# Kernel tuning notes

Measured on AMD Instinct MI355X. Metric: run time of the kernel, lower is better.

## Reference

```python
import jax, jax.numpy as jnp
import numpy as np

IN_DIM = 512
OUT_DIM = 512


def setup_inputs() -> dict:
    key = jax.random.key(0)
    ks = jax.random.split(key, 7)
    B, S = 4, 2048
    scale = 1.0 / np.sqrt(IN_DIM)
    X = jax.random.normal(ks[0], (B, S, IN_DIM), dtype=jnp.float32)
    Wq = jax.random.normal(ks[1], (IN_DIM, OUT_DIM), dtype=jnp.float32) * scale
    Wk = jax.random.normal(ks[2], (IN_DIM, OUT_DIM), dtype=jnp.float32) * scale
    Wv = jax.random.normal(ks[3], (IN_DIM, OUT_DIM), dtype=jnp.float32) * scale
    bq = jnp.zeros((OUT_DIM,), dtype=jnp.float32)
    bk = jnp.zeros((OUT_DIM,), dtype=jnp.float32)
    bv = jnp.zeros((OUT_DIM,), dtype=jnp.float32)
    return {"X": X, "Wq": Wq, "bq": bq, "Wk": Wk, "bk": bk, "Wv": Wv, "bv": bv}


def reference(X, Wq, bq, Wk, bk, Wv, bv):
    # Q/K/V projections: [B,S,in] @ [in,out] -> [B,S,out]
    Q = X @ Wq + bq
    K = X @ Wk + bk
    V = X @ Wv + bv
    d_k = jnp.asarray(Q.shape[-1], Q.dtype)
    # scores: [B,S,S] = QK^T / sqrt(d_k)
    scores = jnp.einsum('bsd,btd->bst', Q, K) / jnp.sqrt(d_k)
    attn = jax.nn.softmax(scores, axis=-1)
    # out: [B,S,out]
    return jnp.einsum('bst,btd->bsd', attn, V)
```

## Files before the change

kernel.cpp:

```cpp
#include <hip/hip_runtime.h>
#include <hip/hip_bf16.h>
#include <stdint.h>

#define SEQ   2048
#define DIM   512
#define BATCH 4

typedef __attribute__((ext_vector_type(8))) short  short8;
typedef __attribute__((ext_vector_type(4))) float  floatx4;

static __device__ __forceinline__ unsigned short f2b(float f) {
  return __builtin_bit_cast(unsigned short, __float2bfloat16(f));
}

static __device__ __forceinline__ void gll16(const void* g, void* l) {
  __builtin_amdgcn_global_load_lds(
      (__attribute__((address_space(1))) void*)(uintptr_t)g,
      (__attribute__((address_space(3))) void*)l, 16, 0, 0);
}


template <int AF, int BF, int WM, int WN, int KC, int PH, int KIT, int NW>
__device__ __forceinline__ void fgemm_p(
    const char* __restrict__ A, int rtA0, int TKA,
    const char* __restrict__ B, int rtB0, int TKB,
    char* lds, floatx4 (&acc)[AF / WM][BF / WN])
{
  constexpr int AWF  = AF / WM, BWF = BF / WN;
  constexpr int SLOT = (AF + BF) * KC * 1024;
  constexpr int L    = KC * (AF / NW + BF / NW);
  constexpr int AC   = AWF / PH;
  static_assert(KIT >= 3, "pipeline needs >=3 K-slots");
  static_assert(AF % NW == 0 && BF % NW == 0, "frag rows must divide waves");
  static_assert(AWF % PH == 0 && L % PH == 0, "phase split must divide");
  const int tid = threadIdx.x;
  const int w = tid >> 6, l = tid & 63;
  const int wm = w % WM, wn = w / WM;

  auto stage_part = [&](char* dst, int kt, int p) {
#pragma unroll
    for (int g = p * (L / PH); g < (p + 1) * (L / PH); ++g) {
      if (g < KC * (AF / NW)) {
        const int c = g / (AF / NW), q = g % (AF / NW);
        const int f = q * NW + w;
        gll16(A + (((size_t)(rtA0 + f) * TKA + kt * KC + c) << 10) + l * 16,
              dst + (c * AF + f) * 1024 + l * 16);
      } else {
        const int h = g - KC * (AF / NW);
        const int c = h / (BF / NW), q = h % (BF / NW);
        const int f = q * NW + w;
        gll16(B + (((size_t)(rtB0 + f) * TKB + kt * KC + c) << 10) + l * 16,
              dst + (KC * AF + c * BF + f) * 1024 + l * 16);
      }
    }
  };

#pragma unroll
  for (int p = 0; p < PH; ++p) stage_part(lds, 0, p);
#pragma unroll
  for (int p = 0; p < PH; ++p) stage_part(lds + SLOT, 1, p);
  asm volatile("s_waitcnt vmcnt(%0) lgkmcnt(0)\ns_barrier" :: "n"(L) : "memory");

  short8 bf[KC][BWF];
  int cs = 0;
#pragma unroll 2
  for (int kt = 0; kt < KIT; ++kt) {
    const char* bA = lds + cs * SLOT;
    const char* bB = bA + KC * AF * 1024;
    int ns = cs - 1; if (ns < 0) ns = 2;
    char* pdst = lds + ns * SLOT;
#pragma unroll
    for (int p = 0; p < PH; ++p) {
      short8 af[KC][AC];
#pragma unroll
      for (int c = 0; c < KC; ++c)
#pragma unroll
        for (int i = 0; i < AC; ++i)
          af[c][i] = *(const short8*)(bA + (c * AF + wm * AWF + p * AC + i) * 1024 + l * 16);
      if (p == 0) {
#pragma unroll
        for (int c = 0; c < KC; ++c)
#pragma unroll
          for (int j = 0; j < BWF; ++j)
            bf[c][j] = *(const short8*)(bB + (c * BF + wn * BWF + j) * 1024 + l * 16);
      }
      if (kt + 2 < KIT) stage_part(pdst, kt + 2, p);

      asm volatile("s_barrier" ::: "memory");
      asm volatile("s_waitcnt lgkmcnt(0)" ::: "memory");
      __builtin_amdgcn_s_setprio(1);
#pragma unroll
      for (int c = 0; c < KC; ++c)
#pragma unroll
        for (int i = 0; i < AC; ++i)
#pragma unroll
          for (int j = 0; j < BWF; ++j)
            acc[p * AC + i][j] = __builtin_amdgcn_mfma_f32_16x16x32_bf16(
                af[c][i], bf[c][j], acc[p * AC + i][j], 0, 0, 0);
      __builtin_amdgcn_s_setprio(0);

      if (p == PH - 1) {
        if (kt + 2 < KIT)
          asm volatile("s_waitcnt vmcnt(%0)\ns_barrier" :: "n"(L) : "memory");
        else if (kt + 1 < KIT)
          asm volatile("s_waitcnt vmcnt(0)\ns_barrier" ::: "memory");
      } else {
        asm volatile("s_barrier" ::: "memory");
      }
    }
    ++cs; if (cs == 3) cs = 0;
  }
}

__global__ __launch_bounds__(256) void setup_kernel(
    const float* __restrict__ X, const float* __restrict__ Wq,
    const float* __restrict__ Wk, const float* __restrict__ Wv,
    short8* __restrict__ XbF, short8* __restrict__ WF)
{
  const int flat = blockIdx.x * 256 + threadIdx.x;
  {
    const int tile = flat >> 6, l = flat & 63;
    const int row = (tile >> 4) * 16 + (l & 15);
    const int k0  = (tile & 15) * 32 + (l >> 4) * 8;
    const float4 v0 = *(const float4*)(X + (size_t)row * DIM + k0);
    const float4 v1 = *(const float4*)(X + (size_t)row * DIM + k0 + 4);
    short8 o;
    o[0] = (short)f2b(v0.x); o[1] = (short)f2b(v0.y);
    o[2] = (short)f2b(v0.z); o[3] = (short)f2b(v0.w);
    o[4] = (short)f2b(v1.x); o[5] = (short)f2b(v1.y);
    o[6] = (short)f2b(v1.z); o[7] = (short)f2b(v1.w);
    XbF[flat] = o;
  }
  if (flat < 3 * 32768) {
    const int z = flat >> 15, within = flat & 32767;
    const float* W = (z == 0) ? Wq : (z == 1) ? Wk : Wv;
    const int tile = within >> 6, l = within & 63;
    const int n  = (tile >> 4) * 16 + (l & 15);
    const int k0 = (tile & 15) * 32 + (l >> 4) * 8;
    short8 o;
#pragma unroll
    for (int e = 0; e < 8; ++e)
      o[e] = (short)f2b(W[(size_t)(k0 + e) * DIM + n]);
    WF[flat] = o;
  }
}

__global__ __launch_bounds__(256, 2) void qkv_kernel(
    const short8* __restrict__ XbF, const short8* __restrict__ WF,
    const float* __restrict__ bq, const float* __restrict__ bk,
    const float* __restrict__ bv,
    unsigned short* __restrict__ QF, unsigned short* __restrict__ KF,
    unsigned short* __restrict__ VF)
{
  __shared__ char lds[73728];
  const int blk = blockIdx.x;
  const int n = (blk & 7) * 48 + (blk >> 3);
  const int lane = threadIdx.x & 63, w = threadIdx.x >> 6;
  const int wm = w & 1, wn = w >> 1;
  const char* Xc = (const char*)XbF;
  const char* Wc = (const char*)WF;
  floatx4 acc[8][4] = {};

  if (n < 256) {
    const int z = n >> 7, y = (n >> 6) & 1, x = n & 63;
    fgemm_p<16, 8, 2, 2, 1, 2, 16, 4>(Wc + (size_t)z * 524288, y * 16, 16,
                                      Xc, x * 8, 16, lds, acc);
    const float* bias = z ? bk : bq;
    unsigned short* OF = z ? KF : QF;
    const int dbase = y * 256 + wm * 128;
    const int sbase = x * 128 + wn * 64;
#pragma unroll
    for (int i2 = 0; i2 < 8; ++i2) {
      const int d0 = dbase + i2 * 16 + (lane >> 4) * 4;
      const float4 b4 = *(const float4*)(bias + d0);
#pragma unroll
      for (int j = 0; j < 4; ++j) {
        const int s = sbase + j * 16 + (lane & 15);
        ushort4 pk;
        pk.x = f2b(acc[i2][j][0] + b4.x);
        pk.y = f2b(acc[i2][j][1] + b4.y);
        pk.z = f2b(acc[i2][j][2] + b4.z);
        pk.w = f2b(acc[i2][j][3] + b4.w);
        *(ushort4*)(OF + (size_t)((s >> 4) * 16 + (d0 >> 5)) * 512 +
                    ((((d0 & 31) >> 3) << 4) | (s & 15)) * 8 + (d0 & 7)) = pk;
      }
    }
  } else {
    const int m = n - 256;
    const int x = m >> 2, y = m & 3;
    fgemm_p<16, 8, 2, 2, 1, 2, 16, 4>(Xc, x * 16, 16,
                                      Wc + 2 * 524288, y * 8, 16, lds, acc);
    const int sbase = x * 256 + wm * 128;
    const int dbase = y * 128 + wn * 64;
#pragma unroll
    for (int i2 = 0; i2 < 8; ++i2) {
      const int s0 = sbase + i2 * 16 + (lane >> 4) * 4;
      const int bt = s0 >> 11, t0 = s0 & 2047;
#pragma unroll
      for (int j = 0; j < 4; ++j) {
        const int d = dbase + j * 16 + (lane & 15);
        const float bn = bv[d];
        ushort4 pk;
        pk.x = f2b(acc[i2][j][0] + bn);
        pk.y = f2b(acc[i2][j][1] + bn);
        pk.z = f2b(acc[i2][j][2] + bn);
        pk.w = f2b(acc[i2][j][3] + bn);
        *(ushort4*)(VF + (size_t)bt * DIM * SEQ +
                    (size_t)((d >> 4) * 64 + (t0 >> 5)) * 512 +
                    ((((t0 & 31) >> 3) << 4) | (d & 15)) * 8 + (t0 & 7)) = pk;
      }
    }
  }
}

__global__ __launch_bounds__(256, 2) void scores_kernel(
    const unsigned short* __restrict__ QF, const unsigned short* __restrict__ KF,
    unsigned short* __restrict__ ScF, float* __restrict__ prow)
{
  __shared__ char lds[73728];
  const int blk = blockIdx.x;
  const int n = (blk & 7) * 64 + (blk >> 3);
  const int b = n >> 7, t = n & 127;
  const int y = t >> 4, x = t & 15;
  const int lane = threadIdx.x & 63, w = threadIdx.x >> 6;
  const int wm = w & 1, wn = w >> 1;
  floatx4 acc[8][4] = {};
  fgemm_p<16, 8, 2, 2, 1, 2, 16, 4>((const char*)KF + (size_t)b * 2097152, y * 16, 16,
                                    (const char*)QF + (size_t)b * 2097152, x * 8, 16,
                                    lds, acc);

  unsigned short* S = ScF + (size_t)b * SEQ * SEQ;
  const float scale = 0.044194173824159216f;
  const int tbase = y * 256 + wm * 128;
  const int sbase = x * 128 + wn * 64;
  float colsum[4] = {0.f, 0.f, 0.f, 0.f};
#pragma unroll
  for (int i2 = 0; i2 < 8; ++i2) {
    const int t0 = tbase + i2 * 16 + (lane >> 4) * 4;
#pragma unroll
    for (int j = 0; j < 4; ++j) {
      const int s = sbase + j * 16 + (lane & 15);
      float e0 = __expf(acc[i2][j][0] * scale);
      float e1 = __expf(acc[i2][j][1] * scale);
      float e2 = __expf(acc[i2][j][2] * scale);
      float e3 = __expf(acc[i2][j][3] * scale);
      colsum[j] += (e0 + e1) + (e2 + e3);
      ushort4 pk;
      pk.x = f2b(e0); pk.y = f2b(e1); pk.z = f2b(e2); pk.w = f2b(e3);
      *(ushort4*)(S + (size_t)((s >> 4) * 64 + (t0 >> 5)) * 512 +
                  ((((t0 & 31) >> 3) << 4) | (s & 15)) * 8 + (t0 & 7)) = pk;
    }
  }
#pragma unroll
  for (int j = 0; j < 4; ++j) {
    colsum[j] += __shfl_xor(colsum[j], 16, 64);
    colsum[j] += __shfl_xor(colsum[j], 32, 64);
  }
  if (lane < 16) {
    float* dst = prow + ((size_t)(y * 2 + wm) * BATCH + b) * SEQ + sbase + lane;
#pragma unroll
    for (int j = 0; j < 4; ++j) dst[j * 16] = colsum[j];
  }
}

__global__ __launch_bounds__(256, 2) void pv_kernel(
    const unsigned short* __restrict__ ScF, const unsigned short* __restrict__ VF,
    const float* __restrict__ prow, float* __restrict__ out)
{
  __shared__ char lds[73728];
  __shared__ float rinv[128];
  const int blk = blockIdx.x;
  const int n = (blk & 7) * 64 + (blk >> 3);
  const int b = n >> 7, r = n & 127;
  const int x = r >> 3, y = r & 7;
  const int t = threadIdx.x;
  if (t < 128) {
    const int s = x * 128 + t;
    float rr = 0.f;
#pragma unroll
    for (int q = 0; q < 16; ++q) rr += prow[((size_t)q * BATCH + b) * SEQ + s];
    rinv[t] = 1.f / rr;
  }
  const int lane = threadIdx.x & 63, w = threadIdx.x >> 6;
  const int wm = w & 1, wn = w >> 1;
  floatx4 acc[4][2] = {};
  fgemm_p<8, 4, 2, 2, 2, 1, 32, 4>((const char*)ScF + (size_t)b * 8388608, x * 8, 64,
                                   (const char*)VF + (size_t)b * 2097152, y * 4, 64,
                                   lds, acc);

  const int mbase = x * 128 + wm * 64;
  const int dbase = y * 64 + wn * 32;
#pragma unroll
  for (int i2 = 0; i2 < 4; ++i2) {
    const int r0 = wm * 64 + i2 * 16 + (lane >> 4) * 4;
    const int m0 = mbase + i2 * 16 + (lane >> 4) * 4;
    const float inv0 = rinv[r0], inv1 = rinv[r0 + 1], inv2 = rinv[r0 + 2], inv3 = rinv[r0 + 3];
#pragma unroll
    for (int j = 0; j < 2; ++j) {
      const int d = dbase + j * 16 + (lane & 15);
      float* o = out + ((size_t)b * SEQ + m0) * DIM + d;
      o[0 * DIM] = acc[i2][j][0] * inv0;
      o[1 * DIM] = acc[i2][j][1] * inv1;
      o[2 * DIM] = acc[i2][j][2] * inv2;
      o[3 * DIM] = acc[i2][j][3] * inv3;
    }
  }
}

extern "C" void kernel_launch(void* const* d_in, const int* in_sizes, int n_in,
                              void* d_out, int out_size, void* d_ws, size_t ws_size,
                              hipStream_t stream) {
  const float* X  = (const float*)d_in[0];
  const float* Wq = (const float*)d_in[1];
  const float* bq = (const float*)d_in[2];
  const float* Wk = (const float*)d_in[3];
  const float* bk = (const float*)d_in[4];
  const float* Wv = (const float*)d_in[5];
  const float* bv = (const float*)d_in[6];
  float* out = (float*)d_out;
  char* ws = (char*)d_ws;

  short8* XbF = (short8*)(ws + 0);
  float*  prow = (float*)(ws + 0);
  short8* WF  = (short8*)(ws + 8388608);
  unsigned short* QF  = (unsigned short*)(ws + 9961472);
  unsigned short* KF  = (unsigned short*)(ws + 18350080);
  unsigned short* VF  = (unsigned short*)(ws + 26738688);
  unsigned short* ScF = (unsigned short*)(ws + 35127296);

  setup_kernel<<<dim3(2048), 256, 0, stream>>>(X, Wq, Wk, Wv, XbF, WF);
  qkv_kernel<<<dim3(384), 256, 0, stream>>>(XbF, WF, bq, bk, bv, QF, KF, VF);
  scores_kernel<<<dim3(512), 256, 0, stream>>>(QF, KF, ScF, prow);
  pv_kernel<<<dim3(512), 256, 0, stream>>>(ScF, VF, prow, out);
}
```

Before: 137.7 us.

## Use eight-wave blocks in all GEMM kernels with per-slot staging

Doubles the waves per block from 4 to 8 in the QKV, scores and PV kernels by splitting the N dimension of each block tile across four wave columns instead of two, which halves each wave's accumulator tile. Staging is restructured so that each wave issues one contiguous share of a whole K slot, all during the first phase, instead of splitting loads across phases. The aim is more waves to hide latency and lower register pressure per wave. The cost is more redundant LDS reads of the A fragments per block, a heavier burst of global loads in phase 0, and an occupancy gain that may be capped by the 72KB of LDS each block uses.

```diff
diff --git a/kernel.cpp b/kernel.cpp
--- a/kernel.cpp
+++ b/kernel.cpp
@@ -21,45 +21,43 @@
 
 
 template <int AF, int BF, int WM, int WN, int KC, int PH, int KIT, int NW>
-__device__ __forceinline__ void fgemm_p(
+__device__ __forceinline__ void fgemm_v2(
     const char* __restrict__ A, int rtA0, int TKA,
     const char* __restrict__ B, int rtB0, int TKB,
     char* lds, floatx4 (&acc)[AF / WM][BF / WN])
 {
   constexpr int AWF  = AF / WM, BWF = BF / WN;
   constexpr int SLOT = (AF + BF) * KC * 1024;
-  constexpr int L    = KC * (AF / NW + BF / NW);
+  constexpr int U    = KC * (AF + BF);
+  constexpr int UW   = U / NW;
   constexpr int AC   = AWF / PH;
   static_assert(KIT >= 3, "pipeline needs >=3 K-slots");
-  static_assert(AF % NW == 0 && BF % NW == 0, "frag rows must divide waves");
-  static_assert(AWF % PH == 0 && L % PH == 0, "phase split must divide");
+  static_assert(U % NW == 0, "stage units must divide waves");
+  static_assert(AWF % PH == 0, "phase split must divide A rows");
   const int tid = threadIdx.x;
   const int w = tid >> 6, l = tid & 63;
   const int wm = w % WM, wn = w / WM;
 
-  auto stage_part = [&](char* dst, int kt, int p) {
-#pragma unroll
-    for (int g = p * (L / PH); g < (p + 1) * (L / PH); ++g) {
-      if (g < KC * (AF / NW)) {
-        const int c = g / (AF / NW), q = g % (AF / NW);
-        const int f = q * NW + w;
+  auto stage_slot = [&](char* dst, int kt) {
+#pragma unroll
+    for (int e = 0; e < UW; ++e) {
+      const int g = w * UW + e;
+      if (g < KC * AF) {
+        const int c = g / AF, f = g % AF;
         gll16(A + (((size_t)(rtA0 + f) * TKA + kt * KC + c) << 10) + l * 16,
               dst + (c * AF + f) * 1024 + l * 16);
       } else {
-        const int h = g - KC * (AF / NW);
-        const int c = h / (BF / NW), q = h % (BF / NW);
-        const int f = q * NW + w;
+        const int h = g - KC * AF;
+        const int c = h / BF, f = h % BF;
         gll16(B + (((size_t)(rtB0 + f) * TKB + kt * KC + c) << 10) + l * 16,
               dst + (KC * AF + c * BF + f) * 1024 + l * 16);
       }
     }
   };
 
-#pragma unroll
-  for (int p = 0; p < PH; ++p) stage_part(lds, 0, p);
-#pragma unroll
-  for (int p = 0; p < PH; ++p) stage_part(lds + SLOT, 1, p);
-  asm volatile("s_waitcnt vmcnt(%0) lgkmcnt(0)\ns_barrier" :: "n"(L) : "memory");
+  stage_slot(lds, 0);
+  stage_slot(lds + SLOT, 1);
+  asm volatile("s_waitcnt vmcnt(%0) lgkmcnt(0)\ns_barrier" :: "n"(UW) : "memory");
 
   short8 bf[KC][BWF];
   int cs = 0;
@@ -83,8 +81,8 @@
 #pragma unroll
           for (int j = 0; j < BWF; ++j)
             bf[c][j] = *(const short8*)(bB + (c * BF + wn * BWF + j) * 1024 + l * 16);
-      }
-      if (kt + 2 < KIT) stage_part(pdst, kt + 2, p);
+        if (kt + 2 < KIT) stage_slot(pdst, kt + 2);
+      }
 
       asm volatile("s_barrier" ::: "memory");
       asm volatile("s_waitcnt lgkmcnt(0)" ::: "memory");
@@ -101,7 +99,7 @@
 
       if (p == PH - 1) {
         if (kt + 2 < KIT)
-          asm volatile("s_waitcnt vmcnt(%0)\ns_barrier" :: "n"(L) : "memory");
+          asm volatile("s_waitcnt vmcnt(%0)\ns_barrier" :: "n"(UW) : "memory");
         else if (kt + 1 < KIT)
           asm volatile("s_waitcnt vmcnt(0)\ns_barrier" ::: "memory");
       } else {
@@ -145,7 +143,7 @@
   }
 }
 
-__global__ __launch_bounds__(256, 2) void qkv_kernel(
+__global__ __launch_bounds__(512, 4) void qkv_kernel(
     const short8* __restrict__ XbF, const short8* __restrict__ WF,
     const float* __restrict__ bq, const float* __restrict__ bk,
     const float* __restrict__ bv,
@@ -159,22 +157,22 @@
   const int wm = w & 1, wn = w >> 1;
   const char* Xc = (const char*)XbF;
   const char* Wc = (const char*)WF;
-  floatx4 acc[8][4] = {};
+  floatx4 acc[8][2] = {};
 
   if (n < 256) {
     const int z = n >> 7, y = (n >> 6) & 1, x = n & 63;
-    fgemm_p<16, 8, 2, 2, 1, 2, 16, 4>(Wc + (size_t)z * 524288, y * 16, 16,
-                                      Xc, x * 8, 16, lds, acc);
+    fgemm_v2<16, 8, 2, 4, 1, 2, 16, 8>(Wc + (size_t)z * 524288, y * 16, 16,
+                                       Xc, x * 8, 16, lds, acc);
     const float* bias = z ? bk : bq;
     unsigned short* OF = z ? KF : QF;
     const int dbase = y * 256 + wm * 128;
-    const int sbase = x * 128 + wn * 64;
+    const int sbase = x * 128 + wn * 32;
 #pragma unroll
     for (int i2 = 0; i2 < 8; ++i2) {
       const int d0 = dbase + i2 * 16 + (lane >> 4) * 4;
       const float4 b4 = *(const float4*)(bias + d0);
 #pragma unroll
-      for (int j = 0; j < 4; ++j) {
+      for (int j = 0; j < 2; ++j) {
         const int s = sbase + j * 16 + (lane & 15);
         ushort4 pk;
         pk.x = f2b(acc[i2][j][0] + b4.x);
@@ -188,16 +186,16 @@
   } else {
     const int m = n - 256;
     const int x = m >> 2, y = m & 3;
-    fgemm_p<16, 8, 2, 2, 1, 2, 16, 4>(Xc, x * 16, 16,
-                                      Wc + 2 * 524288, y * 8, 16, lds, acc);
+    fgemm_v2<16, 8, 2, 4, 1, 2, 16, 8>(Xc, x * 16, 16,
+                                       Wc + 2 * 524288, y * 8, 16, lds, acc);
     const int sbase = x * 256 + wm * 128;
-    const int dbase = y * 128 + wn * 64;
+    const int dbase = y * 128 + wn * 32;
 #pragma unroll
     for (int i2 = 0; i2 < 8; ++i2) {
       const int s0 = sbase + i2 * 16 + (lane >> 4) * 4;
       const int bt = s0 >> 11, t0 = s0 & 2047;
 #pragma unroll
-      for (int j = 0; j < 4; ++j) {
+      for (int j = 0; j < 2; ++j) {
         const int d = dbase + j * 16 + (lane & 15);
         const float bn = bv[d];
         ushort4 pk;
@@ -213,7 +211,7 @@
   }
 }
 
-__global__ __launch_bounds__(256, 2) void scores_kernel(
+__global__ __launch_bounds__(512, 4) void scores_kernel(
     const unsigned short* __restrict__ QF, const unsigned short* __restrict__ KF,
     unsigned short* __restrict__ ScF, float* __restrict__ prow)
 {
@@ -224,21 +222,21 @@
   const int y = t >> 4, x = t & 15;
   const int lane = threadIdx.x & 63, w = threadIdx.x >> 6;
   const int wm = w & 1, wn = w >> 1;
-  floatx4 acc[8][4] = {};
-  fgemm_p<16, 8, 2, 2, 1, 2, 16, 4>((const char*)KF + (size_t)b * 2097152, y * 16, 16,
-                                    (const char*)QF + (size_t)b * 2097152, x * 8, 16,
-                                    lds, acc);
+  floatx4 acc[8][2] = {};
+  fgemm_v2<16, 8, 2, 4, 1, 2, 16, 8>((const char*)KF + (size_t)b * 2097152, y * 16, 16,
+                                     (const char*)QF + (size_t)b * 2097152, x * 8, 16,
+                                     lds, acc);
 
   unsigned short* S = ScF + (size_t)b * SEQ * SEQ;
   const float scale = 0.044194173824159216f;
   const int tbase = y * 256 + wm * 128;
-  const int sbase = x * 128 + wn * 64;
-  float colsum[4] = {0.f, 0.f, 0.f, 0.f};
+  const int sbase = x * 128 + wn * 32;
+  float colsum[2] = {0.f, 0.f};
 #pragma unroll
   for (int i2 = 0; i2 < 8; ++i2) {
     const int t0 = tbase + i2 * 16 + (lane >> 4) * 4;
 #pragma unroll
-    for (int j = 0; j < 4; ++j) {
+    for (int j = 0; j < 2; ++j) {
       const int s = sbase + j * 16 + (lane & 15);
       float e0 = __expf(acc[i2][j][0] * scale);
       float e1 = __expf(acc[i2][j][1] * scale);
@@ -252,18 +250,18 @@
     }
   }
 #pragma unroll
-  for (int j = 0; j < 4; ++j) {
+  for (int j = 0; j < 2; ++j) {
     colsum[j] += __shfl_xor(colsum[j], 16, 64);
     colsum[j] += __shfl_xor(colsum[j], 32, 64);
   }
   if (lane < 16) {
     float* dst = prow + ((size_t)(y * 2 + wm) * BATCH + b) * SEQ + sbase + lane;
 #pragma unroll
-    for (int j = 0; j < 4; ++j) dst[j * 16] = colsum[j];
-  }
-}
-
-__global__ __launch_bounds__(256, 2) void pv_kernel(
+    for (int j = 0; j < 2; ++j) dst[j * 16] = colsum[j];
+  }
+}
+
+__global__ __launch_bounds__(512, 4) void pv_kernel(
     const unsigned short* __restrict__ ScF, const unsigned short* __restrict__ VF,
     const float* __restrict__ prow, float* __restrict__ out)
 {
@@ -283,27 +281,24 @@
   }
   const int lane = threadIdx.x & 63, w = threadIdx.x >> 6;
   const int wm = w & 1, wn = w >> 1;
-  floatx4 acc[4][2] = {};
-  fgemm_p<8, 4, 2, 2, 2, 1, 32, 4>((const char*)ScF + (size_t)b * 8388608, x * 8, 64,
-                                   (const char*)VF + (size_t)b * 2097152, y * 4, 64,
-                                   lds, acc);
+  floatx4 acc[4][1] = {};
+  fgemm_v2<8, 4, 2, 4, 2, 2, 32, 8>((const char*)ScF + (size_t)b * 8388608, x * 8, 64,
+                                    (const char*)VF + (size_t)b * 2097152, y * 4, 64,
+                                    lds, acc);
 
   const int mbase = x * 128 + wm * 64;
-  const int dbase = y * 64 + wn * 32;
+  const int dbase = y * 64 + wn * 16;
 #pragma unroll
   for (int i2 = 0; i2 < 4; ++i2) {
     const int r0 = wm * 64 + i2 * 16 + (lane >> 4) * 4;
     const int m0 = mbase + i2 * 16 + (lane >> 4) * 4;
     const float inv0 = rinv[r0], inv1 = rinv[r0 + 1], inv2 = rinv[r0 + 2], inv3 = rinv[r0 + 3];
-#pragma unroll
-    for (int j = 0; j < 2; ++j) {
-      const int d = dbase + j * 16 + (lane & 15);
-      float* o = out + ((size_t)b * SEQ + m0) * DIM + d;
-      o[0 * DIM] = acc[i2][j][0] * inv0;
-      o[1 * DIM] = acc[i2][j][1] * inv1;
-      o[2 * DIM] = acc[i2][j][2] * inv2;
-      o[3 * DIM] = acc[i2][j][3] * inv3;
-    }
+    const int d = dbase + (lane & 15);
+    float* o = out + ((size_t)b * SEQ + m0) * DIM + d;
+    o[0 * DIM] = acc[i2][0][0] * inv0;
+    o[1 * DIM] = acc[i2][0][1] * inv1;
+    o[2 * DIM] = acc[i2][0][2] * inv2;
+    o[3 * DIM] = acc[i2][0][3] * inv3;
   }
 }
 
@@ -329,7 +324,7 @@
   unsigned short* ScF = (unsigned short*)(ws + 35127296);
 
   setup_kernel<<<dim3(2048), 256, 0, stream>>>(X, Wq, Wk, Wv, XbF, WF);
-  qkv_kernel<<<dim3(384), 256, 0, stream>>>(XbF, WF, bq, bk, bv, QF, KF, VF);
-  scores_kernel<<<dim3(512), 256, 0, stream>>>(QF, KF, ScF, prow);
-  pv_kernel<<<dim3(512), 256, 0, stream>>>(ScF, VF, prow, out);
-}
+  qkv_kernel<<<dim3(384), 512, 0, stream>>>(XbF, WF, bq, bk, bv, QF, KF, VF);
+  scores_kernel<<<dim3(512), 512, 0, stream>>>(QF, KF, ScF, prow);
+  pv_kernel<<<dim3(512), 512, 0, stream>>>(ScF, VF, prow, out);
+}
```

New measurement: 159.7 us. 16.0% more time.
